# Performance work log

Hardware: AMD Instinct MI355X
Metric: run time of the kernel (lower is better)

The kernel has to match this reference:

```python
import jax, jax.numpy as jnp
import numpy as np
from jax import lax

DIM = 1024
N = 8192

def setup_inputs() -> dict:
    key = jax.random.key(0)
    ks = jax.random.split(key, 7)
    ifeats = jax.random.normal(ks[0], (N, DIM), dtype=jnp.float32)
    tfeat_n = jax.random.normal(ks[1], (1, DIM), dtype=jnp.float32)
    tfeat_a = jax.random.normal(ks[2], (1, DIM), dtype=jnp.float32)
    # Conv2d(1, 2, kernel_size=(3,5), padding=(0,2)) params, OIHW
    fan_in_c = 1 * 3 * 5
    bc = 1.0 / np.sqrt(fan_in_c)
    conv_w = jax.random.uniform(ks[3], (2, 1, 3, 5), minval=-bc, maxval=bc, dtype=jnp.float32)
    conv_b = jax.random.uniform(ks[4], (2,), minval=-bc, maxval=bc, dtype=jnp.float32)
    # Linear(2*dim, dim)
    bl = 1.0 / np.sqrt(2 * DIM)
    w2 = jax.random.uniform(ks[5], (DIM, 2 * DIM), minval=-bl, maxval=bl, dtype=jnp.float32)
    b2 = jax.random.uniform(ks[6], (DIM,), minval=-bl, maxval=bl, dtype=jnp.float32)
    return {"ifeats": ifeats, "tfeat_n": tfeat_n, "tfeat_a": tfeat_a,
            "conv_w": conv_w, "conv_b": conv_b, "w2": w2, "b2": b2}

def reference(ifeats, tfeat_n, tfeat_a, conv_w, conv_b, w2, b2):
    n, d = ifeats.shape
    # Batch the per-sample loop: feats_i = [tfeat_n; tfeat_a; ifeats[i]] -> [N,1,3,D]
    tn = jnp.broadcast_to(tfeat_n, (n, d))
    ta = jnp.broadcast_to(tfeat_a, (n, d))
    x1 = jnp.stack([tn, ta, ifeats], axis=1)[:, None]  # [N,1,3,D]
    # Conv2d(1->2, k=(3,5), pad=(0,2)): height collapses 3->1, width D preserved
    x2 = lax.conv_general_dilated(x1, conv_w, window_strides=(1, 1),
                                  padding=((0, 0), (2, 2)),
                                  dimension_numbers=("NCHW", "OIHW", "NCHW"))
    x2 = x2 + conv_b[None, :, None, None]              # [N,2,1,D]
    x2 = jax.nn.gelu(x2, approximate=False)            # torch nn.GELU() is exact
    x2 = x2.reshape(n, 2 * d)                          # channel-major flatten, matches view(1,-1)
    x3 = x2 @ w2.T + b2                                # Linear(2D -> D)
    return ifeats + x3
```

## Files before the change

### kernel.cpp

```cpp
#include <hip/hip_runtime.h>
#include <cstdint>

#define DIMD 1024
#define NROWS 8192
#define KDIM 2048

typedef unsigned short u16;
typedef __bf16 bf16x8 __attribute__((ext_vector_type(8)));
typedef float f32x4 __attribute__((ext_vector_type(4)));

__device__ __forceinline__ u16 f2bf(float f) {
  unsigned u = __builtin_bit_cast(unsigned, f);
  return (u16)((u + 0x7FFFu + ((u >> 16) & 1u)) >> 16);
}

__device__ __forceinline__ float gelu_exact(float x) {
  float s = 0.70710678118654752f * x;
  float a = fabsf(s);
  float k = __fdividef(1.0f, fmaf(0.3275911f, a, 1.0f));
  float p = 1.061405429f;
  p = fmaf(p, k, -1.453152027f);
  p = fmaf(p, k, 1.421413741f);
  p = fmaf(p, k, -0.284496736f);
  p = fmaf(p, k, 0.254829592f);
  p = p * k;
  float e = __expf(-s * s);
  float erf_s = copysignf(fmaf(-p, e, 1.0f), s);
  return 0.5f * x * (1.0f + erf_s);
}

__global__ __launch_bounds__(256) void pre_kernel(
    const float* __restrict__ ifeats, const float* __restrict__ tn,
    const float* __restrict__ ta, const float* __restrict__ cw,
    const float* __restrict__ cb, const float* __restrict__ w2,
    u16* __restrict__ x2, u16* __restrict__ w2b) {
  const int b = blockIdx.x;
  const int t = threadIdx.x;
  if (b < 1024) {
    const int c = t >> 7;
    const int w0 = (t & 127) << 3;
    float cwn[5], cwa[5], cwi[5];
#pragma unroll
    for (int k = 0; k < 5; ++k) {
      cwn[k] = cw[c * 15 + k];
      cwa[k] = cw[c * 15 + 5 + k];
      cwi[k] = cw[c * 15 + 10 + k];
    }
    const float bias = cb[c];
    float base[8];
    {
      float wn[12], wa[12];
#pragma unroll
      for (int j = 0; j < 12; ++j) {
        int wp = w0 - 2 + j;
        bool ok = (wp >= 0) && (wp < DIMD);
        wn[j] = ok ? tn[ok ? wp : 0] : 0.f;
        wa[j] = ok ? ta[ok ? wp : 0] : 0.f;
      }
#pragma unroll
      for (int s = 0; s < 8; ++s) {
        float x = bias;
#pragma unroll
        for (int k = 0; k < 5; ++k) {
          x = fmaf(cwn[k], wn[s + k], x);
          x = fmaf(cwa[k], wa[s + k], x);
        }
        base[s] = x;
      }
    }
    const bool has_l = (w0 > 0);
    const bool has_r = (w0 < DIMD - 8);
#pragma unroll 1
    for (int r = 0; r < 8; ++r) {
      const int row = b * 8 + r;
      const float* irow = ifeats + (size_t)row * DIMD;
      float wi[12];
      float4 m0 = *(const float4*)(irow + w0);
      float4 m1 = *(const float4*)(irow + w0 + 4);
      wi[0] = has_l ? irow[w0 - 2] : 0.f;
      wi[1] = has_l ? irow[w0 - 1] : 0.f;
      wi[2] = m0.x; wi[3] = m0.y; wi[4] = m0.z; wi[5] = m0.w;
      wi[6] = m1.x; wi[7] = m1.y; wi[8] = m1.z; wi[9] = m1.w;
      wi[10] = has_r ? irow[w0 + 8] : 0.f;
      wi[11] = has_r ? irow[w0 + 9] : 0.f;
      union { u16 o[8]; uint4 u; } pk;
#pragma unroll
      for (int s = 0; s < 8; ++s) {
        float x = base[s];
#pragma unroll
        for (int k = 0; k < 5; ++k) x = fmaf(cwi[k], wi[s + k], x);
        pk.o[s] = f2bf(gelu_exact(x));
      }
      *(uint4*)(x2 + (size_t)row * KDIM + c * DIMD + w0) = pk.u;
    }
  } else {
    const int t2 = (b - 1024) * 256 + t;
    const float4* p = (const float4*)(w2 + (size_t)t2 * 8);
    float4 a = p[0], bb = p[1];
    union { u16 o[8]; uint4 v; } pk;
    pk.o[0] = f2bf(a.x);  pk.o[1] = f2bf(a.y);  pk.o[2] = f2bf(a.z);  pk.o[3] = f2bf(a.w);
    pk.o[4] = f2bf(bb.x); pk.o[5] = f2bf(bb.y); pk.o[6] = f2bf(bb.z); pk.o[7] = f2bf(bb.w);
    *(uint4*)(w2b + (size_t)t2 * 8) = pk.v;
  }
}

__device__ __forceinline__ void gl_lds16(const u16* g, u16* l) {
  __builtin_amdgcn_global_load_lds(
      (__attribute__((address_space(1))) void*)g,
      (__attribute__((address_space(3))) void*)l, 16, 0, 0);
}

#define BK 64

__global__ __launch_bounds__(512, 4) void gemm_bt(
    const u16* __restrict__ A,
    const u16* __restrict__ B,
    const float* __restrict__ ifeats,
    const float* __restrict__ b2,
    float* __restrict__ out) {
  constexpr int K = KDIM;
  __shared__ __align__(16) u16 sA[2][128 * BK];
  __shared__ __align__(16) u16 sB[2][128 * BK];

  const int tid = threadIdx.x;
  const int wv = tid >> 6;
  const int lane = tid & 63;
  const int id = blockIdx.x;
  const int xcd = id & 7;
  const int s_ = id >> 3;
  const int i0 = (xcd * 8 + (s_ >> 3)) * 128;
  const int j0 = (s_ & 7) * 128;

  const int wm = (wv & 1) * 64;
  const int wn = (wv >> 1) * 32;
  const int quad = lane >> 4;
  const int r16 = lane & 15;
  const int sw = r16 & 7;

  const int srow = lane >> 3;
  const int schunk = (lane & 7) ^ srow;
  const u16* gA[2];
  const u16* gB[2];
#pragma unroll
  for (int i = 0; i < 2; ++i) {
    int r = wv * 16 + i * 8 + srow;
    gA[i] = A + (size_t)(i0 + r) * K + schunk * 8;
    gB[i] = B + (size_t)(j0 + r) * K + schunk * 8;
  }

  const f32x4 vzero = {0.f, 0.f, 0.f, 0.f};
  f32x4 acc[4][2];
#pragma unroll
  for (int a = 0; a < 4; ++a)
#pragma unroll
    for (int b = 0; b < 2; ++b) acc[a][b] = vzero;

  auto stage = [&](int buf, int k0) {
#pragma unroll
    for (int i = 0; i < 2; ++i) {
      u16* la = &sA[buf][(wv * 16 + i * 8) * BK];
      u16* lb = &sB[buf][(wv * 16 + i * 8) * BK];
      gl_lds16(gA[i] + k0, la);
      gl_lds16(gB[i] + k0, lb);
    }
  };

  auto compute = [&](int buf) {
#pragma unroll
    for (int s = 0; s < 2; ++s) {
      bf16x8 av[4], bv[2];
#pragma unroll
      for (int mt = 0; mt < 4; ++mt)
        av[mt] = *(const bf16x8*)&sA[buf][(wm + mt * 16 + r16) * BK + (((s * 4 + quad) ^ sw) << 3)];
#pragma unroll
      for (int nt = 0; nt < 2; ++nt)
        bv[nt] = *(const bf16x8*)&sB[buf][(wn + nt * 16 + r16) * BK + (((s * 4 + quad) ^ sw) << 3)];
#pragma unroll
      for (int mt = 0; mt < 4; ++mt)
#pragma unroll
        for (int nt = 0; nt < 2; ++nt)
          acc[mt][nt] = __builtin_amdgcn_mfma_f32_16x16x32_bf16(av[mt], bv[nt], acc[mt][nt], 0, 0, 0);
    }
  };

  stage(0, 0);
  for (int k0 = 0; k0 < K; k0 += 2 * BK) {
    __syncthreads();
    if (k0 + BK < K) stage(1, k0 + BK);
    compute(0);
    __syncthreads();
    if (k0 + 2 * BK < K) stage(0, k0 + 2 * BK);
    compute(1);
  }

#pragma unroll
  for (int nt = 0; nt < 2; ++nt) {
    int col = j0 + wn + nt * 16 + r16;
    float bias = b2[col];
#pragma unroll
    for (int mt = 0; mt < 4; ++mt) {
      int rbase = i0 + wm + mt * 16 + quad * 4;
#pragma unroll
      for (int r = 0; r < 4; ++r) {
        size_t idx = (size_t)(rbase + r) * DIMD + col;
        out[idx] = ifeats[idx] + bias + acc[mt][nt][r];
      }
    }
  }
}

extern "C" void kernel_launch(void* const* d_in, const int* in_sizes, int n_in,
                              void* d_out, int out_size, void* d_ws, size_t ws_size,
                              hipStream_t stream) {
  const float* ifeats = (const float*)d_in[0];
  const float* tn     = (const float*)d_in[1];
  const float* ta     = (const float*)d_in[2];
  const float* cw     = (const float*)d_in[3];
  const float* cb     = (const float*)d_in[4];
  const float* w2     = (const float*)d_in[5];
  const float* b2     = (const float*)d_in[6];
  float* out = (float*)d_out;

  u16* w2b = (u16*)d_ws;
  u16* x2  = (u16*)((char*)d_ws + (size_t)DIMD * KDIM * 2);

  pre_kernel<<<2048, 256, 0, stream>>>(ifeats, tn, ta, cw, cb, w2, x2, w2b);
  gemm_bt<<<512, 512, 0, stream>>>(x2, w2b, ifeats, b2, out);
}
```

Before: 158.0 us.

## Enlarge GEMM tile to 256x128 with triple-buffered LDS and interleaved prefetch

The GEMM block tile grows from 128x128 to 256x128, and the grid shrinks to 256 blocks with one resident block per CU. LDS becomes triple-buffered, with async global-to-LDS prefetches two tiles ahead issued between split MFMA phases. Explicit vmcnt waits, s_barrier, sched_barrier and setprio replace __syncthreads. The aim is more data reuse per LDS load and better hiding of load latency, at the cost of lower occupancy. With only 256 blocks, some of the 256 CUs may sit idle, and tile imbalance becomes a risk.

```diff
diff --git a/kernel.cpp b/kernel.cpp
--- a/kernel.cpp
+++ b/kernel.cpp
@@ -111,16 +111,19 @@
 }
 
 #define BK 64
-
-__global__ __launch_bounds__(512, 4) void gemm_bt(
+#define BM 256
+#define BN 128
+#define NTILE 32
+
+__global__ __launch_bounds__(512, 1) void gemm_bt(
     const u16* __restrict__ A,
     const u16* __restrict__ B,
     const float* __restrict__ ifeats,
     const float* __restrict__ b2,
     float* __restrict__ out) {
   constexpr int K = KDIM;
-  __shared__ __align__(16) u16 sA[2][128 * BK];
-  __shared__ __align__(16) u16 sB[2][128 * BK];
+  __shared__ __align__(16) u16 sA[3][BM * BK];
+  __shared__ __align__(16) u16 sB[3][BN * BK];
 
   const int tid = threadIdx.x;
   const int wv = tid >> 6;
@@ -128,73 +131,107 @@
   const int id = blockIdx.x;
   const int xcd = id & 7;
   const int s_ = id >> 3;
-  const int i0 = (xcd * 8 + (s_ >> 3)) * 128;
-  const int j0 = (s_ & 7) * 128;
-
-  const int wm = (wv & 1) * 64;
-  const int wn = (wv >> 1) * 32;
+  const int i0 = (xcd * 4 + (s_ >> 3)) * BM;
+  const int j0 = (s_ & 7) * BN;
+
+  const int wm = (wv >> 1) * 64;
+  const int wn = (wv & 1) * 64;
   const int quad = lane >> 4;
   const int r16 = lane & 15;
   const int sw = r16 & 7;
 
   const int srow = lane >> 3;
   const int schunk = (lane & 7) ^ srow;
-  const u16* gA[2];
+  const u16* gA[4];
   const u16* gB[2];
 #pragma unroll
-  for (int i = 0; i < 2; ++i) {
-    int r = wv * 16 + i * 8 + srow;
-    gA[i] = A + (size_t)(i0 + r) * K + schunk * 8;
-    gB[i] = B + (size_t)(j0 + r) * K + schunk * 8;
+  for (int u = 0; u < 4; ++u)
+    gA[u] = A + (size_t)(i0 + wv * 32 + u * 8 + srow) * K + schunk * 8;
+#pragma unroll
+  for (int u = 0; u < 2; ++u)
+    gB[u] = B + (size_t)(j0 + wv * 16 + u * 8 + srow) * K + schunk * 8;
+
+  const f32x4 vzero = {0.f, 0.f, 0.f, 0.f};
+  f32x4 acc[4][4];
+#pragma unroll
+  for (int a = 0; a < 4; ++a)
+#pragma unroll
+    for (int b = 0; b < 4; ++b) acc[a][b] = vzero;
+
+  u16* pa0 = (u16*)sA[0]; u16* pa1 = (u16*)sA[1]; u16* pa2 = (u16*)sA[2];
+  u16* pb0 = (u16*)sB[0]; u16* pb1 = (u16*)sB[1]; u16* pb2 = (u16*)sB[2];
+
+  auto issueA = [&](u16* buf, int t) {
+#pragma unroll
+    for (int u = 0; u < 4; ++u)
+      gl_lds16(gA[u] + t * BK, buf + (wv * 32 + u * 8) * BK);
+  };
+  auto issueB = [&](u16* buf, int t) {
+#pragma unroll
+    for (int u = 0; u < 2; ++u)
+      gl_lds16(gB[u] + t * BK, buf + (wv * 16 + u * 8) * BK);
+  };
+  auto rdfrag = [&](const u16* buf, int row, int ks) -> bf16x8 {
+    return *(const bf16x8*)&buf[(row + r16) * BK + (((ks * 4 + quad) ^ sw) << 3)];
+  };
+
+  issueA(pa0, 0); issueB(pb0, 0);
+  issueA(pa1, 1); issueB(pb1, 1);
+  asm volatile("s_waitcnt vmcnt(6)" ::: "memory");
+  __builtin_amdgcn_s_barrier();
+  __builtin_amdgcn_sched_barrier(0);
+
+  for (int t = 0; t < NTILE; ++t) {
+    const bool pf = (t + 2) < NTILE;
+    bf16x8 av[2][2], bv[4][2];
+#pragma unroll
+    for (int mt = 0; mt < 2; ++mt)
+#pragma unroll
+      for (int ks = 0; ks < 2; ++ks) av[mt][ks] = rdfrag(pa0, wm + mt * 16, ks);
+#pragma unroll
+    for (int nt = 0; nt < 4; ++nt)
+#pragma unroll
+      for (int ks = 0; ks < 2; ++ks) bv[nt][ks] = rdfrag(pb0, wn + nt * 16, ks);
+    if (pf) issueA(pa2, t + 2);
+    __builtin_amdgcn_s_barrier();
+    __builtin_amdgcn_sched_barrier(0);
+    __builtin_amdgcn_s_setprio(1);
+#pragma unroll
+    for (int ks = 0; ks < 2; ++ks)
+#pragma unroll
+      for (int mt = 0; mt < 2; ++mt)
+#pragma unroll
+        for (int nt = 0; nt < 4; ++nt)
+          acc[mt][nt] = __builtin_amdgcn_mfma_f32_16x16x32_bf16(av[mt][ks], bv[nt][ks], acc[mt][nt], 0, 0, 0);
+    __builtin_amdgcn_s_setprio(0);
+    bf16x8 aw[2][2];
+#pragma unroll
+    for (int mt = 0; mt < 2; ++mt)
+#pragma unroll
+      for (int ks = 0; ks < 2; ++ks) aw[mt][ks] = rdfrag(pa0, wm + (mt + 2) * 16, ks);
+    if (pf) issueB(pb2, t + 2);
+    __builtin_amdgcn_s_barrier();
+    __builtin_amdgcn_sched_barrier(0);
+    __builtin_amdgcn_s_setprio(1);
+#pragma unroll
+    for (int ks = 0; ks < 2; ++ks)
+#pragma unroll
+      for (int mt = 0; mt < 2; ++mt)
+#pragma unroll
+        for (int nt = 0; nt < 4; ++nt)
+          acc[mt + 2][nt] = __builtin_amdgcn_mfma_f32_16x16x32_bf16(aw[mt][ks], bv[nt][ks], acc[mt + 2][nt], 0, 0, 0);
+    __builtin_amdgcn_s_setprio(0);
+    if (pf) asm volatile("s_waitcnt vmcnt(6)" ::: "memory");
+    else    asm volatile("s_waitcnt vmcnt(0)" ::: "memory");
+    __builtin_amdgcn_s_barrier();
+    __builtin_amdgcn_sched_barrier(0);
+    u16* x;
+    x = pa0; pa0 = pa1; pa1 = pa2; pa2 = x;
+    x = pb0; pb0 = pb1; pb1 = pb2; pb2 = x;
   }
 
-  const f32x4 vzero = {0.f, 0.f, 0.f, 0.f};
-  f32x4 acc[4][2];
-#pragma unroll
-  for (int a = 0; a < 4; ++a)
-#pragma unroll
-    for (int b = 0; b < 2; ++b) acc[a][b] = vzero;
-
-  auto stage = [&](int buf, int k0) {
-#pragma unroll
-    for (int i = 0; i < 2; ++i) {
-      u16* la = &sA[buf][(wv * 16 + i * 8) * BK];
-      u16* lb = &sB[buf][(wv * 16 + i * 8) * BK];
-      gl_lds16(gA[i] + k0, la);
-      gl_lds16(gB[i] + k0, lb);
-    }
-  };
-
-  auto compute = [&](int buf) {
-#pragma unroll
-    for (int s = 0; s < 2; ++s) {
-      bf16x8 av[4], bv[2];
-#pragma unroll
-      for (int mt = 0; mt < 4; ++mt)
-        av[mt] = *(const bf16x8*)&sA[buf][(wm + mt * 16 + r16) * BK + (((s * 4 + quad) ^ sw) << 3)];
-#pragma unroll
-      for (int nt = 0; nt < 2; ++nt)
-        bv[nt] = *(const bf16x8*)&sB[buf][(wn + nt * 16 + r16) * BK + (((s * 4 + quad) ^ sw) << 3)];
-#pragma unroll
-      for (int mt = 0; mt < 4; ++mt)
-#pragma unroll
-        for (int nt = 0; nt < 2; ++nt)
-          acc[mt][nt] = __builtin_amdgcn_mfma_f32_16x16x32_bf16(av[mt], bv[nt], acc[mt][nt], 0, 0, 0);
-    }
-  };
-
-  stage(0, 0);
-  for (int k0 = 0; k0 < K; k0 += 2 * BK) {
-    __syncthreads();
-    if (k0 + BK < K) stage(1, k0 + BK);
-    compute(0);
-    __syncthreads();
-    if (k0 + 2 * BK < K) stage(0, k0 + 2 * BK);
-    compute(1);
-  }
-
-#pragma unroll
-  for (int nt = 0; nt < 2; ++nt) {
+#pragma unroll
+  for (int nt = 0; nt < 4; ++nt) {
     int col = j0 + wn + nt * 16 + r16;
     float bias = b2[col];
 #pragma unroll
@@ -225,5 +262,5 @@
   u16* x2  = (u16*)((char*)d_ws + (size_t)DIMD * KDIM * 2);
 
   pre_kernel<<<2048, 256, 0, stream>>>(ifeats, tn, ta, cw, cb, w2, x2, w2b);
-  gemm_bt<<<512, 512, 0, stream>>>(x2, w2b, ifeats, b2, out);
-}
+  gemm_bt<<<256, 512, 0, stream>>>(x2, w2b, ifeats, b2, out);
+}
```

After: 155.0 us. Within noise of the previous version (-1.9%).

## Restructure GEMM: 4 waves with 64x64 tiles, B from global into registers

Applied to the files above, without the earlier changes.

The GEMM now runs 256 threads per block instead of 512, so each wave computes a 64x64 output tile. Only A is staged through LDS via global_load_lds. B fragments are read straight from global memory into registers and double-buffered one k-tile ahead. The loop uses manual vmcnt waits, s_setprio around the MFMA bursts and a single barrier per iteration. This aims to halve LDS traffic and barriers and to overlap loads with MFMA, at the cost of more registers, uncoalesced per-lane B loads and fewer waves for hiding latency.

```diff
diff --git a/kernel.cpp b/kernel.cpp
--- a/kernel.cpp
+++ b/kernel.cpp
@@ -111,16 +111,44 @@
 }
 
 #define BK 64
-
-__global__ __launch_bounds__(512, 4) void gemm_bt(
+#define NTILE 32
+
+#define GITER(T, BUFC, BUFN, CUR, NXT)                                         \
+  {                                                                            \
+    bf16x8 av[4][2];                                                           \
+    _Pragma("unroll") for (int mt = 0; mt < 4; ++mt)                           \
+      _Pragma("unroll") for (int ks = 0; ks < 2; ++ks)                         \
+        av[mt][ks] = *(const bf16x8*)&BUFC[(wm + mt * 16 + r16) * BK +         \
+                                           (((ks * 4 + quad) ^ sw) << 3)];     \
+    _Pragma("unroll") for (int nt = 0; nt < 4; ++nt) pB[nt] += BK;             \
+    if ((T) + 1 < NTILE) {                                                     \
+      _Pragma("unroll") for (int u = 0; u < 4; ++u)                            \
+        gl_lds16(gA[u] + ((T) + 1) * BK, BUFN + (wv * 32 + u * 8) * BK);       \
+      _Pragma("unroll") for (int nt = 0; nt < 4; ++nt)                         \
+        _Pragma("unroll") for (int ks = 0; ks < 2; ++ks)                       \
+          NXT[nt][ks] = *(const bf16x8*)(pB[nt] + ks * 32);                    \
+    }                                                                          \
+    __builtin_amdgcn_s_setprio(1);                                             \
+    _Pragma("unroll") for (int ks = 0; ks < 2; ++ks)                           \
+      _Pragma("unroll") for (int mt = 0; mt < 4; ++mt)                         \
+        _Pragma("unroll") for (int nt = 0; nt < 4; ++nt)                       \
+          acc[mt][nt] = __builtin_amdgcn_mfma_f32_16x16x32_bf16(               \
+              av[mt][ks], CUR[nt][ks], acc[mt][nt], 0, 0, 0);                  \
+    __builtin_amdgcn_s_setprio(0);                                             \
+    asm volatile("s_waitcnt vmcnt(8)" ::: "memory");                           \
+    __builtin_amdgcn_s_barrier();                                              \
+    __builtin_amdgcn_sched_barrier(0);                                         \
+  }
+
+__global__ __launch_bounds__(256, 2) void gemm_bt(
     const u16* __restrict__ A,
     const u16* __restrict__ B,
     const float* __restrict__ ifeats,
     const float* __restrict__ b2,
     float* __restrict__ out) {
   constexpr int K = KDIM;
-  __shared__ __align__(16) u16 sA[2][128 * BK];
-  __shared__ __align__(16) u16 sB[2][128 * BK];
+  __shared__ __align__(16) u16 sA0[128 * BK];
+  __shared__ __align__(16) u16 sA1[128 * BK];
 
   const int tid = threadIdx.x;
   const int wv = tid >> 6;
@@ -132,69 +160,51 @@
   const int j0 = (s_ & 7) * 128;
 
   const int wm = (wv & 1) * 64;
-  const int wn = (wv >> 1) * 32;
+  const int wn = (wv >> 1) * 64;
   const int quad = lane >> 4;
   const int r16 = lane & 15;
   const int sw = r16 & 7;
 
   const int srow = lane >> 3;
   const int schunk = (lane & 7) ^ srow;
-  const u16* gA[2];
-  const u16* gB[2];
-#pragma unroll
-  for (int i = 0; i < 2; ++i) {
-    int r = wv * 16 + i * 8 + srow;
-    gA[i] = A + (size_t)(i0 + r) * K + schunk * 8;
-    gB[i] = B + (size_t)(j0 + r) * K + schunk * 8;
-  }
+  const u16* gA[4];
+#pragma unroll
+  for (int u = 0; u < 4; ++u)
+    gA[u] = A + (size_t)(i0 + wv * 32 + u * 8 + srow) * K + schunk * 8;
+
+  const u16* pB[4];
+#pragma unroll
+  for (int nt = 0; nt < 4; ++nt)
+    pB[nt] = B + (size_t)(j0 + wn + nt * 16 + r16) * K + quad * 8;
 
   const f32x4 vzero = {0.f, 0.f, 0.f, 0.f};
-  f32x4 acc[4][2];
+  f32x4 acc[4][4];
 #pragma unroll
   for (int a = 0; a < 4; ++a)
 #pragma unroll
-    for (int b = 0; b < 2; ++b) acc[a][b] = vzero;
-
-  auto stage = [&](int buf, int k0) {
-#pragma unroll
-    for (int i = 0; i < 2; ++i) {
-      u16* la = &sA[buf][(wv * 16 + i * 8) * BK];
-      u16* lb = &sB[buf][(wv * 16 + i * 8) * BK];
-      gl_lds16(gA[i] + k0, la);
-      gl_lds16(gB[i] + k0, lb);
-    }
-  };
-
-  auto compute = [&](int buf) {
-#pragma unroll
-    for (int s = 0; s < 2; ++s) {
-      bf16x8 av[4], bv[2];
-#pragma unroll
-      for (int mt = 0; mt < 4; ++mt)
-        av[mt] = *(const bf16x8*)&sA[buf][(wm + mt * 16 + r16) * BK + (((s * 4 + quad) ^ sw) << 3)];
-#pragma unroll
-      for (int nt = 0; nt < 2; ++nt)
-        bv[nt] = *(const bf16x8*)&sB[buf][(wn + nt * 16 + r16) * BK + (((s * 4 + quad) ^ sw) << 3)];
-#pragma unroll
-      for (int mt = 0; mt < 4; ++mt)
-#pragma unroll
-        for (int nt = 0; nt < 2; ++nt)
-          acc[mt][nt] = __builtin_amdgcn_mfma_f32_16x16x32_bf16(av[mt], bv[nt], acc[mt][nt], 0, 0, 0);
-    }
-  };
-
-  stage(0, 0);
-  for (int k0 = 0; k0 < K; k0 += 2 * BK) {
-    __syncthreads();
-    if (k0 + BK < K) stage(1, k0 + BK);
-    compute(0);
-    __syncthreads();
-    if (k0 + 2 * BK < K) stage(0, k0 + 2 * BK);
-    compute(1);
-  }
-
-#pragma unroll
-  for (int nt = 0; nt < 2; ++nt) {
+    for (int b = 0; b < 4; ++b) acc[a][b] = vzero;
+
+  bf16x8 bvX[4][2], bvY[4][2];
+
+#pragma unroll
+  for (int u = 0; u < 4; ++u)
+    gl_lds16(gA[u], sA0 + (wv * 32 + u * 8) * BK);
+#pragma unroll
+  for (int nt = 0; nt < 4; ++nt)
+#pragma unroll
+    for (int ks = 0; ks < 2; ++ks)
+      bvX[nt][ks] = *(const bf16x8*)(pB[nt] + ks * 32);
+  asm volatile("s_waitcnt vmcnt(8)" ::: "memory");
+  __builtin_amdgcn_s_barrier();
+  __builtin_amdgcn_sched_barrier(0);
+
+  for (int t = 0; t < NTILE; t += 2) {
+    GITER(t,     sA0, sA1, bvX, bvY);
+    GITER(t + 1, sA1, sA0, bvY, bvX);
+  }
+
+#pragma unroll
+  for (int nt = 0; nt < 4; ++nt) {
     int col = j0 + wn + nt * 16 + r16;
     float bias = b2[col];
 #pragma unroll
@@ -225,5 +235,5 @@
   u16* x2  = (u16*)((char*)d_ws + (size_t)DIMD * KDIM * 2);
 
   pre_kernel<<<2048, 256, 0, stream>>>(ifeats, tn, ta, cw, cb, w2, x2, w2b);
-  gemm_bt<<<512, 512, 0, stream>>>(x2, w2b, ifeats, b2, out);
-}
+  gemm_bt<<<512, 256, 0, stream>>>(x2, w2b, ifeats, b2, out);
+}
```

After: 189.4 us. 19.9% more time.
